# Performance work log

Measured on AMD Instinct MI355X. Metric: run time of the kernel, lower is better.

Reference implementation:

```python
import jax, jax.numpy as jnp
import numpy as np

EPS = 1e-8


def setup_inputs() -> dict:
    key0 = jax.random.key(0)
    k1, k2, k3 = jax.random.split(key0, 3)
    B, Q, K, H, D = 8, 16, 65536, 1, 64
    query = jax.random.normal(k1, (B, Q, H, D), dtype=jnp.float32)
    key = jax.random.normal(k2, (B, K, H, D), dtype=jnp.float32)
    value = jax.random.normal(k3, (B, K, H, D), dtype=jnp.float32)
    return {"query": query, "key": key, "value": value}


def reference(query, key, value):
    # query: [B, Q, H, D]; key/value: [B, K, H, D]
    qk_features = query.shape[-1]
    q = query * (1.0 / np.sqrt(qk_features)).astype(np.float32)
    # scores: [B, H, Q, K]
    attn = jnp.einsum('bqhd,bkhd->bhqk', q, key)
    # inverted attention: softmax over the QUERY axis (-2)
    attn = jax.nn.softmax(attn, axis=-2)
    # renormalize over keys ('mean' norm_type)
    normalizer = jnp.sum(attn, axis=-1, keepdims=True) + EPS
    attn_n = attn / normalizer
    # updates: [B, Q, H, D]
    updates = jnp.einsum('bhqk,bkhd->bqhd', attn_n, value)
    # num_heads == 1 -> squeeze head dim: [B, Q, D]
    output = jnp.squeeze(updates, axis=-2)
    return (output, attn)
```

## Files before the change

### kernel.cpp

```cpp
#include <hip/hip_runtime.h>

#define KTOT 65536
#define QN 16
#define DN 64
#define BN 8
#define TILE 256

#define QS_OFF 0
#define R0_OFF 1024
#define R1_OFF 5120
#define SMEM_FLOATS 9216

__device__ __forceinline__ void gload_lds16(const float* g, float* l)
{
    __builtin_amdgcn_global_load_lds(
        (const __attribute__((address_space(1))) void*)g,
        (__attribute__((address_space(3))) void*)l, 16, 0, 0);
}

#define WAIT_VM(N)  do { asm volatile("s_waitcnt vmcnt(" #N ")" ::: "memory");      \
                         __builtin_amdgcn_sched_barrier(0); } while (0)
#define LGKM0()     do { asm volatile("s_waitcnt lgkmcnt(0)" ::: "memory");         \
                         __builtin_amdgcn_sched_barrier(0); } while (0)

#define STAGE_WV(RX, kb4, qo4)                                                      \
    {                                                                               \
        _Pragma("unroll")                                                           \
        for (int j = 0; j < 4; ++j) {                                               \
            const int r_ = (wv << 6) + (j << 4) + (lane >> 2);                      \
            const int p_ = (lane & 3) ^ ((r_ >> 1) & 3);                            \
            gload_lds16((const float*)((kb4) + r_ * 16 + (qo4) + p_),               \
                        (float*)(((float4*)&smem[RX]) + ((wv << 8) + (j << 6) + lane))); \
        }                                                                           \
    }

#define DOT_Q(qt, RX)                                                               \
    {                                                                               \
        _Pragma("unroll")                                                           \
        for (int cc = 0; cc < 4; ++cc) {                                            \
            const float4 kv = ((const float4*)&smem[RX])[tid * 4 + (cc ^ fr)];      \
            _Pragma("unroll")                                                       \
            for (int q = 0; q < QN; ++q) {                                          \
                const float4 qv = *reinterpret_cast<const float4*>(                 \
                    &smem[QS_OFF + q * DN + (qt) * 16 + cc * 4]);                   \
                s[q] = fmaf(kv.x, qv.x, s[q]);                                      \
                s[q] = fmaf(kv.y, qv.y, s[q]);                                      \
                s[q] = fmaf(kv.z, qv.z, s[q]);                                      \
                s[q] = fmaf(kv.w, qv.w, s[q]);                                      \
            }                                                                       \
        }                                                                           \
    }

__global__ __launch_bounds__(256, 4) void fused_attn(
    const float* __restrict__ query, const float* __restrict__ key,
    const float* __restrict__ value, float* __restrict__ attn,
    float* __restrict__ upart, int NCH, int ntiles)
{
    __shared__ float smem[SMEM_FLOATS];
    const int b    = blockIdx.y;
    const int c    = blockIdx.x;
    const int tid  = threadIdx.x;
    const int wv   = tid >> 6;
    const int lane = tid & 63;
    const int chunk = ntiles * TILE;
    const int fr   = (tid >> 1) & 3;
    const int AW   = R1_OFF + wv * (QN * 64);

    {
        float4 qv = reinterpret_cast<const float4*>(query + (size_t)b * QN * DN)[tid];
        qv.x *= 0.125f; qv.y *= 0.125f; qv.z *= 0.125f; qv.w *= 0.125f;
        reinterpret_cast<float4*>(&smem[QS_OFF])[tid] = qv;
    }
    __syncthreads();

    {
        const float4* kb4 = reinterpret_cast<const float4*>(
            key + ((size_t)b * KTOT + c * chunk) * DN);
        STAGE_WV(R0_OFF, kb4, 0);
        STAGE_WV(R1_OFF, kb4, 4);
        __builtin_amdgcn_sched_barrier(0);
    }

    float U[QN];
    #pragma unroll
    for (int q = 0; q < QN; ++q) U[q] = 0.f;

    for (int t = 0; t < ntiles; ++t) {
        const int krow0 = c * chunk + t * TILE;
        const float4* kb4  = reinterpret_cast<const float4*>(
            key + ((size_t)b * KTOT + krow0) * DN);
        const float4* kb4n = kb4 + TILE * 16;
        const float*  vptr = value + ((size_t)b * KTOT + krow0 + wv * 64) * DN + lane;

        float s[QN];
        #pragma unroll
        for (int q = 0; q < QN; ++q) s[q] = 0.f;

        WAIT_VM(4);
        DOT_Q(0, R0_OFF);
        LGKM0(); STAGE_WV(R0_OFF, kb4, 8);
        __builtin_amdgcn_sched_barrier(0);

        WAIT_VM(4);
        DOT_Q(1, R1_OFF);
        LGKM0(); STAGE_WV(R1_OFF, kb4, 12);
        __builtin_amdgcn_sched_barrier(0);

        WAIT_VM(4);
        DOT_Q(2, R0_OFF);

        float va[8];
        #pragma unroll
        for (int i = 0; i < 8; ++i) va[i] = vptr[(size_t)i * DN];
        __builtin_amdgcn_sched_barrier(0);
        WAIT_VM(8);
        DOT_Q(3, R1_OFF);

        float m = s[0];
        #pragma unroll
        for (int q = 1; q < QN; ++q) m = fmaxf(m, s[q]);
        float sum = 0.f;
        #pragma unroll
        for (int q = 0; q < QN; ++q) { s[q] = __expf(s[q] - m); sum += s[q]; }
        const float inv = 1.0f / sum;
        {
            float* ab = attn + (size_t)b * QN * KTOT + krow0 + tid;
            #pragma unroll
            for (int q = 0; q < QN; ++q) {
                const float a = s[q] * inv;
                __builtin_nontemporal_store(a, ab + (size_t)q * KTOT);
                smem[AW + q * 64 + lane] = a;
            }
        }

        #pragma unroll 1
        for (int kk = 0; kk < 64; kk += 8) {
            float vb[8];
            const int nxt = kk + 8;
            if (nxt < 64) {
                #pragma unroll
                for (int i = 0; i < 8; ++i) vb[i] = vptr[(size_t)(nxt + i) * DN];
            }
            #pragma unroll
            for (int kq = 0; kq < 8; kq += 4) {
                #pragma unroll
                for (int q = 0; q < QN; ++q) {
                    const float4 av = *reinterpret_cast<const float4*>(
                        &smem[AW + q * 64 + kk + kq]);
                    U[q] = fmaf(av.x, va[kq + 0], U[q]);
                    U[q] = fmaf(av.y, va[kq + 1], U[q]);
                    U[q] = fmaf(av.z, va[kq + 2], U[q]);
                    U[q] = fmaf(av.w, va[kq + 3], U[q]);
                }
            }
            #pragma unroll
            for (int i = 0; i < 8; ++i) va[i] = vb[i];
        }

        if (t + 1 < ntiles) {
            LGKM0();
            STAGE_WV(R0_OFF, kb4n, 0);
            STAGE_WV(R1_OFF, kb4n, 4);
            __builtin_amdgcn_sched_barrier(0);
        }
    }

    __syncthreads();
    #pragma unroll
    for (int q = 0; q < QN; ++q)
        smem[R0_OFF + (wv * QN + q) * DN + lane] = U[q];
    __syncthreads();

    {
        const int q = tid >> 4, d0 = (tid & 15) * 4;
        const float4 r0 = *reinterpret_cast<const float4*>(&smem[R0_OFF + (0 * QN + q) * DN + d0]);
        const float4 r1 = *reinterpret_cast<const float4*>(&smem[R0_OFF + (1 * QN + q) * DN + d0]);
        const float4 r2 = *reinterpret_cast<const float4*>(&smem[R0_OFF + (2 * QN + q) * DN + d0]);
        const float4 r3 = *reinterpret_cast<const float4*>(&smem[R0_OFF + (3 * QN + q) * DN + d0]);
        float4 rs;
        rs.x = r0.x + r1.x + r2.x + r3.x;
        rs.y = r0.y + r1.y + r2.y + r3.y;
        rs.z = r0.z + r1.z + r2.z + r3.z;
        rs.w = r0.w + r1.w + r2.w + r3.w;
        *reinterpret_cast<float4*>(
            &upart[(((size_t)b * NCH + c) * QN + q) * DN + d0]) = rs;
    }
}

__global__ __launch_bounds__(256) void k3_fin(
    const float* __restrict__ attn, const float* __restrict__ upart,
    float* __restrict__ out, int NCH)
{
    const int b = blockIdx.x, q = blockIdx.y;
    const int tid = threadIdx.x;
    const int wv = tid >> 6, lane = tid & 63;

    const float4* ap = reinterpret_cast<const float4*>(attn + ((size_t)b * QN + q) * KTOT);
    float nv = 0.f;
    #pragma unroll 4
    for (int i = tid; i < KTOT / 4; i += 256) {
        const float4 a = ap[i];
        nv += (a.x + a.y) + (a.z + a.w);
    }
    #pragma unroll
    for (int off = 1; off < 64; off <<= 1) nv += __shfl_xor(nv, off, 64);
    __shared__ float nred[4];
    if (lane == 0) nred[wv] = nv;

    float acc = 0.f;
    for (int c = wv; c < NCH; c += 4)
        acc += upart[(((size_t)b * NCH + c) * QN + q) * DN + lane];
    __shared__ float ured[4][DN];
    ured[wv][lane] = acc;
    __syncthreads();

    if (tid < DN) {
        const float n   = nred[0] + nred[1] + nred[2] + nred[3];
        const float inv = 1.0f / (n + 1e-8f);
        const float u   = ured[0][tid] + ured[1][tid] + ured[2][tid] + ured[3][tid];
        out[((size_t)b * QN + q) * DN + tid] = u * inv;
    }
}

extern "C" void kernel_launch(void* const* d_in, const int* in_sizes, int n_in,
                              void* d_out, int out_size, void* d_ws, size_t ws_size,
                              hipStream_t stream)
{
    const float* query = (const float*)d_in[0];
    const float* key   = (const float*)d_in[1];
    const float* value = (const float*)d_in[2];

    float* out  = (float*)d_out;
    float* attn = (float*)d_out + (size_t)BN * QN * DN;

    int NCH = 128;
    while (NCH > 8 && (size_t)BN * NCH * QN * DN * 4 > ws_size) NCH >>= 1;
    const int ntiles = (KTOT / NCH) / TILE;

    float* upart = (float*)d_ws;

    fused_attn<<<dim3(NCH, BN), 256, 0, stream>>>(query, key, value, attn,
                                                  upart, NCH, ntiles);
    k3_fin   <<<dim3(BN, QN), 256, 0, stream>>>(attn, upart, out, NCH);
}
```

Measured before the change: 83.36 us.

## Split value accumulation so each lane computes two d-columns over half the keys

Reorganizes the attn·V accumulation so each wave's two half-waves cover 32 keys each, and each lane holds two output columns (d and d+32). Every attention value read from LDS now feeds two FMAs, halving LDS reads per FMA in the update loop. The cost is twice the accumulator registers, which is why launch bounds drop from 4 to 3 waves per EU. The epilogue reduction is reworked to sum 8 partials in two passes, adding syncs.

```diff
diff --git a/kernel.cpp b/kernel.cpp
--- a/kernel.cpp
+++ b/kernel.cpp
@@ -51,7 +51,7 @@
         }                                                                           \
     }
 
-__global__ __launch_bounds__(256, 4) void fused_attn(
+__global__ __launch_bounds__(256, 3) void fused_attn(
     const float* __restrict__ query, const float* __restrict__ key,
     const float* __restrict__ value, float* __restrict__ attn,
     float* __restrict__ upart, int NCH, int ntiles)
@@ -65,6 +65,9 @@
     const int chunk = ntiles * TILE;
     const int fr   = (tid >> 1) & 3;
     const int AW   = R1_OFF + wv * (QN * 64);
+    const int g    = lane >> 5;
+    const int dd   = lane & 31;
+    const int AK   = AW + g * 32;
 
     {
         float4 qv = reinterpret_cast<const float4*>(query + (size_t)b * QN * DN)[tid];
@@ -81,16 +84,16 @@
         __builtin_amdgcn_sched_barrier(0);
     }
 
-    float U[QN];
-    #pragma unroll
-    for (int q = 0; q < QN; ++q) U[q] = 0.f;
+    float U0[QN], U1[QN];
+    #pragma unroll
+    for (int q = 0; q < QN; ++q) { U0[q] = 0.f; U1[q] = 0.f; }
 
     for (int t = 0; t < ntiles; ++t) {
         const int krow0 = c * chunk + t * TILE;
         const float4* kb4  = reinterpret_cast<const float4*>(
             key + ((size_t)b * KTOT + krow0) * DN);
         const float4* kb4n = kb4 + TILE * 16;
-        const float*  vptr = value + ((size_t)b * KTOT + krow0 + wv * 64) * DN + lane;
+        const float*  vptr = value + ((size_t)b * KTOT + krow0 + wv * 64 + g * 32) * DN + dd;
 
         float s[QN];
         #pragma unroll
@@ -109,11 +112,14 @@
         WAIT_VM(4);
         DOT_Q(2, R0_OFF);
 
-        float va[8];
-        #pragma unroll
-        for (int i = 0; i < 8; ++i) va[i] = vptr[(size_t)i * DN];
-        __builtin_amdgcn_sched_barrier(0);
-        WAIT_VM(8);
+        float va0[8], va1[8];
+        #pragma unroll
+        for (int i = 0; i < 8; ++i) {
+            va0[i] = vptr[(size_t)i * DN];
+            va1[i] = vptr[(size_t)i * DN + 32];
+        }
+        __builtin_amdgcn_sched_barrier(0);
+        WAIT_VM(16);
         DOT_Q(3, R1_OFF);
 
         float m = s[0];
@@ -134,27 +140,34 @@
         }
 
         #pragma unroll 1
-        for (int kk = 0; kk < 64; kk += 8) {
-            float vb[8];
+        for (int kk = 0; kk < 32; kk += 8) {
+            float vb0[8], vb1[8];
             const int nxt = kk + 8;
-            if (nxt < 64) {
+            if (nxt < 32) {
                 #pragma unroll
-                for (int i = 0; i < 8; ++i) vb[i] = vptr[(size_t)(nxt + i) * DN];
+                for (int i = 0; i < 8; ++i) {
+                    vb0[i] = vptr[(size_t)(nxt + i) * DN];
+                    vb1[i] = vptr[(size_t)(nxt + i) * DN + 32];
+                }
             }
             #pragma unroll
             for (int kq = 0; kq < 8; kq += 4) {
                 #pragma unroll
                 for (int q = 0; q < QN; ++q) {
                     const float4 av = *reinterpret_cast<const float4*>(
-                        &smem[AW + q * 64 + kk + kq]);
-                    U[q] = fmaf(av.x, va[kq + 0], U[q]);
-                    U[q] = fmaf(av.y, va[kq + 1], U[q]);
-                    U[q] = fmaf(av.z, va[kq + 2], U[q]);
-                    U[q] = fmaf(av.w, va[kq + 3], U[q]);
+                        &smem[AK + q * 64 + kk + kq]);
+                    U0[q] = fmaf(av.x, va0[kq + 0], U0[q]);
+                    U1[q] = fmaf(av.x, va1[kq + 0], U1[q]);
+                    U0[q] = fmaf(av.y, va0[kq + 1], U0[q]);
+                    U1[q] = fmaf(av.y, va1[kq + 1], U1[q]);
+                    U0[q] = fmaf(av.z, va0[kq + 2], U0[q]);
+                    U1[q] = fmaf(av.z, va1[kq + 2], U1[q]);
+                    U0[q] = fmaf(av.w, va0[kq + 3], U0[q]);
+                    U1[q] = fmaf(av.w, va1[kq + 3], U1[q]);
                 }
             }
             #pragma unroll
-            for (int i = 0; i < 8; ++i) va[i] = vb[i];
+            for (int i = 0; i < 8; ++i) { va0[i] = vb0[i]; va1[i] = vb1[i]; }
         }
 
         if (t + 1 < ntiles) {
@@ -166,24 +179,39 @@
     }
 
     __syncthreads();
+    const int p = (wv << 1) + g;
     #pragma unroll
     for (int q = 0; q < QN; ++q)
-        smem[R0_OFF + (wv * QN + q) * DN + lane] = U[q];
-    __syncthreads();
-
-    {
-        const int q = tid >> 4, d0 = (tid & 15) * 4;
-        const float4 r0 = *reinterpret_cast<const float4*>(&smem[R0_OFF + (0 * QN + q) * DN + d0]);
-        const float4 r1 = *reinterpret_cast<const float4*>(&smem[R0_OFF + (1 * QN + q) * DN + d0]);
-        const float4 r2 = *reinterpret_cast<const float4*>(&smem[R0_OFF + (2 * QN + q) * DN + d0]);
-        const float4 r3 = *reinterpret_cast<const float4*>(&smem[R0_OFF + (3 * QN + q) * DN + d0]);
-        float4 rs;
-        rs.x = r0.x + r1.x + r2.x + r3.x;
-        rs.y = r0.y + r1.y + r2.y + r3.y;
-        rs.z = r0.z + r1.z + r2.z + r3.z;
-        rs.w = r0.w + r1.w + r2.w + r3.w;
-        *reinterpret_cast<float4*>(
-            &upart[(((size_t)b * NCH + c) * QN + q) * DN + d0]) = rs;
+        smem[R0_OFF + (p * QN + q) * 32 + dd] = U0[q];
+    __syncthreads();
+    {
+        const int q  = tid >> 4;
+        const int d0 = (tid & 15) * 2;
+        float s0 = 0.f, s1 = 0.f;
+        #pragma unroll
+        for (int pp = 0; pp < 8; ++pp) {
+            s0 += smem[R0_OFF + (pp * QN + q) * 32 + d0];
+            s1 += smem[R0_OFF + (pp * QN + q) * 32 + d0 + 1];
+        }
+        upart[(((size_t)b * NCH + c) * QN + q) * DN + d0]     = s0;
+        upart[(((size_t)b * NCH + c) * QN + q) * DN + d0 + 1] = s1;
+    }
+    __syncthreads();
+    #pragma unroll
+    for (int q = 0; q < QN; ++q)
+        smem[R0_OFF + (p * QN + q) * 32 + dd] = U1[q];
+    __syncthreads();
+    {
+        const int q  = tid >> 4;
+        const int d0 = (tid & 15) * 2;
+        float s0 = 0.f, s1 = 0.f;
+        #pragma unroll
+        for (int pp = 0; pp < 8; ++pp) {
+            s0 += smem[R0_OFF + (pp * QN + q) * 32 + d0];
+            s1 += smem[R0_OFF + (pp * QN + q) * 32 + d0 + 1];
+        }
+        upart[(((size_t)b * NCH + c) * QN + q) * DN + 32 + d0]     = s0;
+        upart[(((size_t)b * NCH + c) * QN + q) * DN + 32 + d0 + 1] = s1;
     }
 }
 
```

Result: slower. 91.58 us (+9.9%).
